# Performance work log

Hardware: AMD Instinct MI355X
Metric: run time of the kernel (lower is better)

## Reference

```python
import jax, jax.numpy as jnp
import numpy as np

T = 4096
V = 88   # visible_dim
H = 512  # hidden_dim
R = 512  # rnn_hidden_dim
REG_FACTOR = 0.2
GIBBS_STEPS = 20
EPS = 1e-6


def setup_inputs() -> dict:
    key = jax.random.key(0)
    ks = jax.random.split(key, 8)
    scale = 1.0 / np.sqrt(H)
    return {
        "visible": (jax.random.uniform(ks[0], (T, V)) < 0.5).astype(jnp.float32),
        "rand_h": jax.random.uniform(ks[1], (T - 1, GIBBS_STEPS, H), dtype=jnp.float32),
        "rand_v": jax.random.uniform(ks[2], (T - 1, GIBBS_STEPS, V), dtype=jnp.float32),
        "w": jax.random.normal(ks[3], (H, V), dtype=jnp.float32) * scale,
        "wuu": jax.random.normal(ks[4], (R, R), dtype=jnp.float32) * scale,
        "wuv": jax.random.normal(ks[5], (V, R), dtype=jnp.float32) * scale,
        "wuh": jax.random.normal(ks[6], (H, R), dtype=jnp.float32) * scale,
        "wvu": jax.random.normal(ks[7], (R, V), dtype=jnp.float32) * scale,
        "bv": jnp.zeros((V,), jnp.float32),
        "bh": jnp.zeros((H,), jnp.float32),
        "bu": jnp.zeros((R,), jnp.float32),
        "u0": jnp.zeros((R,), jnp.float32),
    }


def reference(visible, rand_h, rand_v, w, wuu, wuv, wuh, wvu, bv, bh, bu, u0):
    time_steps = visible.shape[0]
    v_seq = visible[1:]  # v_t for t = 1..T-1, shape [T-1, V]

    # RNN state depends only on data, not on Gibbs samples -> single scan.
    def u_step(u_prev, v_t):
        u_new = jnp.tanh(wvu @ v_t + wuu @ u_prev + bu)
        return u_new, u_prev  # emit u_{t-1} (bias conditioning state)

    _, u_prev = jax.lax.scan(u_step, u0, v_seq)  # [T-1, R]

    # Per-timestep RBM biases (F.linear(u, W, b) = u @ W.T + b).
    bh_t = u_prev @ wuh.T + bh  # [T-1, H]
    bv_t = u_prev @ wuv.T + bv  # [T-1, V]

    # 20 Gibbs steps, batched over all time steps at once.
    def gibbs_step(v, rands):
        rh, rv = rands  # [T-1, H], [T-1, V]
        p_h = jax.nn.sigmoid(v @ w.T + bh_t)
        h = jax.nn.relu(jnp.sign(p_h - rh))         # Bernoulli sample
        p_v = jax.nn.sigmoid(h @ w + bv_t)
        v_new = jax.nn.relu(jnp.sign(p_v - rv))
        return v_new, None

    neg, _ = jax.lax.scan(
        gibbs_step, v_seq,
        (jnp.swapaxes(rand_h, 0, 1), jnp.swapaxes(rand_v, 0, 1)),
    )  # negative samples [T-1, V]

    # Cross-entropy between data and sigmoid(bv_t), summed then /time_steps.
    y_t = jax.nn.sigmoid(bv_t)
    total_cost = jnp.sum(
        -v_seq * jnp.log(EPS + y_t) - (1.0 - v_seq) * jnp.log(EPS + 1.0 - y_t)
    ) / time_steps

    reg_term = (jnp.linalg.norm(wuv) + jnp.linalg.norm(wuh)) * REG_FACTOR
    total_cost = total_cost + reg_term

    mse = jnp.mean(jnp.abs(v_seq - neg), axis=1)  # per-timestep, [T-1]
    return total_cost, mse, reg_term
```

## Files before the change

kernel.cpp:

```cpp
#include <hip/hip_runtime.h>
#include <cstdint>
#include <cstddef>

#define T4096 4096
#define TM1 4095
#define NV 88
#define NH 512
#define NR 512
#define GS 20
#define EPSV 1e-6f

#define U_OFF 0
#define AB_OFF 2096640
#define BV_OFF 4193280
#define SC_OFF 4553640

__device__ __forceinline__ unsigned int agent_load_u32(const unsigned int* p) {
  return __hip_atomic_load(p, __ATOMIC_RELAXED, __HIP_MEMORY_SCOPE_AGENT);
}
__device__ __forceinline__ void agent_store_f32(float* p, float v) {
  __hip_atomic_store(p, v, __ATOMIC_RELAXED, __HIP_MEMORY_SCOPE_AGENT);
}
__device__ __forceinline__ float sigmoidf_(float x) {
  return 1.0f / (1.0f + expf(-x));
}

__device__ __forceinline__ void store_sc0(float* p, float v) {
  asm volatile("global_store_dword %0, %1, off sc0" :: "v"(p), "v"(v) : "memory");
}
__device__ __forceinline__ unsigned load_sc0(const unsigned* p) {
  unsigned r;
  asm volatile("global_load_dword %0, %1, off sc0\n\ts_waitcnt vmcnt(0)"
               : "=v"(r) : "v"(p) : "memory");
  return r;
}

__device__ __forceinline__ unsigned poll_stag_sc0(const unsigned* p) {
  unsigned r0, r1, r2, r3;
  asm volatile(
    "Lp%=:\n\t"
    "global_load_dword %0, %4, off sc0\n\t"
    "s_sleep 1\n\t"
    "global_load_dword %1, %4, off sc0\n\t"
    "s_sleep 1\n\t"
    "global_load_dword %2, %4, off sc0\n\t"
    "s_sleep 1\n\t"
    "global_load_dword %3, %4, off sc0\n\t"
    "s_waitcnt vmcnt(0)\n\t"
    "v_cmp_ne_u32 vcc, -1, %0\n\t"
    "v_cndmask_b32 %3, %3, %0, vcc\n\t"
    "v_cmp_ne_u32 vcc, -1, %1\n\t"
    "v_cndmask_b32 %3, %3, %1, vcc\n\t"
    "v_cmp_ne_u32 vcc, -1, %2\n\t"
    "v_cndmask_b32 %3, %3, %2, vcc\n\t"
    "v_cmp_eq_u32 vcc, -1, %3\n\t"
    "s_cbranch_vccnz Lp%=\n\t"
    : "=&v"(r0), "=&v"(r1), "=&v"(r2), "=&v"(r3)
    : "v"(p) : "vcc", "memory");
  return r3;
}
__device__ __forceinline__ unsigned poll_stag_sys(const unsigned* p) {
  unsigned r0, r1, r2, r3;
  asm volatile(
    "Lq%=:\n\t"
    "global_load_dword %0, %4, off sc0 sc1\n\t"
    "s_sleep 1\n\t"
    "global_load_dword %1, %4, off sc0 sc1\n\t"
    "s_sleep 1\n\t"
    "global_load_dword %2, %4, off sc0 sc1\n\t"
    "s_sleep 1\n\t"
    "global_load_dword %3, %4, off sc0 sc1\n\t"
    "s_waitcnt vmcnt(0)\n\t"
    "v_cmp_ne_u32 vcc, -1, %0\n\t"
    "v_cndmask_b32 %3, %3, %0, vcc\n\t"
    "v_cmp_ne_u32 vcc, -1, %1\n\t"
    "v_cndmask_b32 %3, %3, %1, vcc\n\t"
    "v_cmp_ne_u32 vcc, -1, %2\n\t"
    "v_cndmask_b32 %3, %3, %2, vcc\n\t"
    "v_cmp_eq_u32 vcc, -1, %3\n\t"
    "s_cbranch_vccnz Lq%=\n\t"
    : "=&v"(r0), "=&v"(r1), "=&v"(r2), "=&v"(r3)
    : "v"(p) : "vcc", "memory");
  return r3;
}

__global__ __launch_bounds__(256) void k_a(const float* __restrict__ visible,
                                           const float* __restrict__ wvu,
                                           const float* __restrict__ bu,
                                           float* __restrict__ A) {
  __shared__ float vbuf[NV * 8];
  const int tid = threadIdx.x;
  const int t0 = blockIdx.x * 8;
  for (int idx = tid; idx < NV * 8; idx += 256) {
    int j = idx / NV, v = idx - j * NV;
    int t = t0 + j;
    vbuf[v * 8 + j] = (t < TM1) ? visible[(size_t)(t + 1) * NV + v] : 0.f;
  }
  __syncthreads();
  for (int rr = 0; rr < 2; rr++) {
    int r = tid + rr * 256;
    float b0 = bu[r];
    float acc[8];
#pragma unroll
    for (int j = 0; j < 8; j++) acc[j] = b0;
    const float* wr = wvu + (size_t)r * NV;
    for (int v = 0; v < NV; v++) {
      float wv = wr[v];
#pragma unroll
      for (int j = 0; j < 8; j++) acc[j] = fmaf(wv, vbuf[v * 8 + j], acc[j]);
    }
#pragma unroll
    for (int j = 0; j < 8; j++) {
      int t = t0 + j;
      if (t < TM1) A[(size_t)t * NR + r] = acc[j];
    }
  }
}

__global__ __launch_bounds__(256) void k_r(const float* __restrict__ wuv,
                                           const float* __restrict__ wuh,
                                           float* __restrict__ sc) {
  size_t stride = (size_t)gridDim.x * 256;
  size_t gid = (size_t)blockIdx.x * 256 + threadIdx.x;
  float s1 = 0.f, s2 = 0.f;
  for (size_t i = gid; i < (size_t)NV * NR; i += stride) { float x = wuv[i]; s1 = fmaf(x, x, s1); }
  for (size_t i = gid; i < (size_t)NH * NR; i += stride) { float x = wuh[i]; s2 = fmaf(x, x, s2); }
  for (int off = 32; off > 0; off >>= 1) {
    s1 += __shfl_down(s1, off, 64);
    s2 += __shfl_down(s2, off, 64);
  }
  if ((threadIdx.x & 63) == 0) {
    atomicAdd(&sc[1], s1);
    atomicAdd(&sc[2], s2);
  }
}

__global__ __launch_bounds__(1024, 4) void k_u5(const float* __restrict__ wuu,
                                                const float* __restrict__ A,
                                                const float* __restrict__ u0,
                                                float* __restrict__ U,
                                                unsigned* __restrict__ ub) {
  __shared__ int s_slot;
  __shared__ int s_fast;
  __shared__ float u_lds[NR];
  __shared__ float partials[1024];
  const int tid = threadIdx.x;
  unsigned* claimc = ub + 8;
  unsigned* winner = ub + 16;
  unsigned* hs     = ub + 17;
  unsigned* vd     = ub + 33;

  if (tid == 0) {
    unsigned xcd;
    asm volatile("s_getreg_b32 %0, hwreg(HW_REG_XCC_ID, 0, 4)" : "=s"(xcd));
    xcd &= 7u;
    unsigned c = atomicAdd(&claimc[xcd], 1u);
    int slot = -1;
    if (c < 4u) {
      if (c == 3u) atomicCAS(winner, 0xFFFFFFFFu, xcd);
      unsigned wnr;
      do { wnr = agent_load_u32(winner); } while (wnr == 0xFFFFFFFFu);
      if (wnr == xcd) slot = (int)c;
    }
    s_slot = slot;
  }
  __syncthreads();
  const int slot = s_slot;
  if (slot < 0) return;

  if (tid == 0) {
    int fast = 1;
    for (int round = 0; round < 4 && fast; ++round) {
      unsigned* hw = hs + round * 4;
      store_sc0((float*)&hw[slot], 0.0f);
      for (int o = 0; o < 4; ++o) {
        if (o == slot) continue;
        int ok = 0;
        for (int it = 0; it < 300; ++it) {
          if (load_sc0(&hw[o]) != 0xFFFFFFFFu) { ok = 1; break; }
        }
        if (!ok) fast = 0;
      }
    }
    __hip_atomic_store(&vd[slot], (unsigned)(fast ? 1 : 0),
                       __ATOMIC_RELAXED, __HIP_MEMORY_SCOPE_AGENT);
    for (int o = 0; o < 4; ++o) {
      unsigned v;
      do { v = agent_load_u32(&vd[o]); } while (v == 0xFFFFFFFFu);
      if (v != 1u) fast = 0;
    }
    s_fast = fast;
  }
  __syncthreads();
  const int fast = s_fast;

  const int r_loc = tid & 127;
  const int kc = tid >> 7;
  const int r0 = slot * 128;

  float Wreg[64];
  {
    const float* wr = wuu + (size_t)(r0 + r_loc) * NR + kc * 64;
#pragma unroll
    for (int i = 0; i < 16; i++) ((float4*)Wreg)[i] = ((const float4*)wr)[i];
  }
#pragma unroll
  for (int i = 0; i < 64; i++) asm volatile("" : "+v"(Wreg[i]));

  if (tid < NR) u_lds[tid] = u0[tid];
  if (tid < 128) agent_store_f32(&U[r0 + tid], u0[r0 + tid]);
  float a_cur = (tid < 128) ? A[r0 + tid] : 0.f;
  int pword = -1;
  if (tid >= 128 && tid < 512) {
    int p = tid - 128;
    pword = (p < r0) ? p : p + 128;
  }
  __syncthreads();

  for (int t = 1; t <= TM1 - 1; t++) {
    float acc = 0.f;
    const float* uc = u_lds + kc * 64;
#pragma unroll
    for (int i = 0; i < 64; i += 4) {
      float4 uv = *(const float4*)(uc + i);
      acc = fmaf(Wreg[i],     uv.x, acc);
      acc = fmaf(Wreg[i + 1], uv.y, acc);
      acc = fmaf(Wreg[i + 2], uv.z, acc);
      acc = fmaf(Wreg[i + 3], uv.w, acc);
    }
    partials[kc * 128 + r_loc] = acc;
    __syncthreads();
    if (tid < 128) {
      float s = a_cur;
#pragma unroll
      for (int kk = 0; kk < 8; kk++) s += partials[kk * 128 + tid];
      float val = tanhf(s);
      if (fast) store_sc0(&U[(size_t)t * NR + r0 + tid], val);
      else      agent_store_f32(&U[(size_t)t * NR + r0 + tid], val);
      u_lds[r0 + tid] = val;
      a_cur = A[(size_t)t * NR + r0 + tid];
    } else if (pword >= 0) {
      const unsigned* p = (const unsigned*)(U + (size_t)t * NR) + pword;
      unsigned w = fast ? poll_stag_sc0(p) : poll_stag_sys(p);
      u_lds[pword] = __uint_as_float(w);
    }
    __syncthreads();
  }
}

__global__ __launch_bounds__(256) void k_bh(const float* __restrict__ Uu,
                                            const float* __restrict__ wuh,
                                            const float* __restrict__ wuv,
                                            const float* __restrict__ bh,
                                            const float* __restrict__ bv,
                                            const float* __restrict__ visible,
                                            float* __restrict__ bht,
                                            float* __restrict__ bvt,
                                            float* __restrict__ sc) {
  __shared__ float uT[NR * 20];
  __shared__ float red[256];
  const int tid = threadIdx.x;
  const int t0 = blockIdx.x * 16;
  const int nt = min(16, TM1 - t0);
  for (int idx = tid; idx < 16 * NR; idx += 256) {
    int tt = idx >> 9, k = idx & 511;
    uT[k * 20 + tt] = (tt < nt) ? Uu[(size_t)(t0 + tt) * NR + k] : 0.f;
  }
  __syncthreads();
  const int h1 = tid, h2 = tid + 256;
  const bool hasv = tid < NV;
  float acc1[16], acc2[16], accv[16];
#pragma unroll
  for (int i = 0; i < 16; i++) acc1[i] = acc2[i] = accv[i] = 0.f;
  const float* w1p = wuh + (size_t)h1 * NR;
  const float* w2p = wuh + (size_t)h2 * NR;
  const float* wvp = wuv + (size_t)(hasv ? tid : 0) * NR;
  for (int k = 0; k < NR; k++) {
    float u16[16];
#pragma unroll
    for (int q = 0; q < 4; q++) *(float4*)(u16 + 4 * q) = *(const float4*)(uT + k * 20 + 4 * q);
    float a = w1p[k], b = w2p[k];
    float c = hasv ? wvp[k] : 0.f;
#pragma unroll
    for (int i = 0; i < 16; i++) {
      acc1[i] = fmaf(a, u16[i], acc1[i]);
      acc2[i] = fmaf(b, u16[i], acc2[i]);
      accv[i] = fmaf(c, u16[i], accv[i]);
    }
  }
  float bh1 = bh[h1], bh2 = bh[h2];
#pragma unroll
  for (int i = 0; i < 16; i++) {
    if (i < nt) {
      bht[(size_t)(t0 + i) * NH + h1] = acc1[i] + bh1;
      bht[(size_t)(t0 + i) * NH + h2] = acc2[i] + bh2;
    }
  }
  float ce = 0.f;
  if (hasv) {
    float bvv = bv[tid];
    for (int i = 0; i < nt; i++) {
      float x = accv[i] + bvv;
      bvt[(size_t)(t0 + i) * NV + tid] = x;
      float y = sigmoidf_(x);
      float vs = visible[(size_t)(t0 + i + 1) * NV + tid];
      ce += -vs * logf(EPSV + y) - (1.f - vs) * logf(EPSV + 1.f - y);
    }
  }
  red[tid] = ce;
  __syncthreads();
  for (int s = 128; s > 0; s >>= 1) {
    if (tid < s) red[tid] += red[tid + s];
    __syncthreads();
  }
  if (tid == 0) atomicAdd(&sc[0], red[0]);
}

__global__ __launch_bounds__(256) void k_g(const float* __restrict__ w,
                                           const float* __restrict__ visible,
                                           const float* __restrict__ rand_h,
                                           const float* __restrict__ rand_v,
                                           const float* __restrict__ bht,
                                           const float* __restrict__ bvt,
                                           float* __restrict__ out) {
  __shared__ float vlds[NV * 20];
  __shared__ float hlds[NH * 20];
  const int tid = threadIdx.x;
  const int t0 = blockIdx.x * 16;
  const int nt = min(16, TM1 - t0);
  for (int idx = tid; idx < NV * 16; idx += 256) {
    int j = idx / NV, v = idx - j * NV;
    vlds[v * 20 + j] = (j < nt) ? visible[(size_t)(t0 + j + 1) * NV + v] : 0.f;
  }
  for (int idx = tid; idx < NH * 20; idx += 256) hlds[idx] = 0.f;
  __syncthreads();
  const int h1 = tid, h2 = tid + 256;
  const int tg = tid >> 5, vg = tid & 31;
  const int v0 = vg * 4;
  const bool bact = vg < 22;
  for (int k = 0; k < GS; k++) {
    {
      float acc1[16], acc2[16];
#pragma unroll
      for (int i = 0; i < 16; i++) acc1[i] = acc2[i] = 0.f;
      const float* w1p = w + (size_t)h1 * NV;
      const float* w2p = w + (size_t)h2 * NV;
      for (int v = 0; v < NV; v++) {
        float vv[16];
#pragma unroll
        for (int q = 0; q < 4; q++) *(float4*)(vv + 4 * q) = *(const float4*)(vlds + v * 20 + 4 * q);
        float a = w1p[v], b = w2p[v];
#pragma unroll
        for (int i = 0; i < 16; i++) {
          acc1[i] = fmaf(a, vv[i], acc1[i]);
          acc2[i] = fmaf(b, vv[i], acc2[i]);
        }
      }
#pragma unroll
      for (int i = 0; i < 16; i++) {
        if (i < nt) {
          size_t t = (size_t)(t0 + i);
          float x1 = acc1[i] + bht[t * NH + h1];
          float x2 = acc2[i] + bht[t * NH + h2];
          float p1 = sigmoidf_(x1);
          float p2 = sigmoidf_(x2);
          float r1 = rand_h[(t * GS + k) * NH + h1];
          float r2 = rand_h[(t * GS + k) * NH + h2];
          hlds[h1 * 20 + i] = (p1 > r1) ? 1.f : 0.f;
          hlds[h2 * 20 + i] = (p2 > r2) ? 1.f : 0.f;
        }
      }
    }
    __syncthreads();
    if (bact) {
      float acc[2][4];
#pragma unroll
      for (int a = 0; a < 2; a++)
#pragma unroll
        for (int b = 0; b < 4; b++) acc[a][b] = 0.f;
#pragma unroll 4
      for (int h = 0; h < NH; h++) {
        float2 hv = *(const float2*)(hlds + h * 20 + tg * 2);
        float4 w4 = *(const float4*)(w + (size_t)h * NV + v0);
        acc[0][0] = fmaf(hv.x, w4.x, acc[0][0]);
        acc[0][1] = fmaf(hv.x, w4.y, acc[0][1]);
        acc[0][2] = fmaf(hv.x, w4.z, acc[0][2]);
        acc[0][3] = fmaf(hv.x, w4.w, acc[0][3]);
        acc[1][0] = fmaf(hv.y, w4.x, acc[1][0]);
        acc[1][1] = fmaf(hv.y, w4.y, acc[1][1]);
        acc[1][2] = fmaf(hv.y, w4.z, acc[1][2]);
        acc[1][3] = fmaf(hv.y, w4.w, acc[1][3]);
      }
#pragma unroll
      for (int a = 0; a < 2; a++) {
        int tt = tg * 2 + a;
        if (tt < nt) {
          size_t t = (size_t)(t0 + tt);
#pragma unroll
          for (int i = 0; i < 4; i++) {
            int v = v0 + i;
            float x = acc[a][i] + bvt[t * NV + v];
            float p = sigmoidf_(x);
            float r = rand_v[(t * GS + k) * NV + v];
            vlds[v * 20 + tt] = (p > r) ? 1.f : 0.f;
          }
        }
      }
    }
    __syncthreads();
  }
  if (tid < 16 && tid < nt) {
    int tt = tid;
    float s = 0.f;
    for (int v = 0; v < NV; v++) {
      float vs = visible[(size_t)(t0 + tt + 1) * NV + v];
      s += fabsf(vs - vlds[v * 20 + tt]);
    }
    out[1 + t0 + tt] = s / 88.f;
  }
}

__global__ void k_f(const float* __restrict__ sc, float* __restrict__ out) {
  float reg = 0.2f * (sqrtf(sc[1]) + sqrtf(sc[2]));
  out[0] = sc[0] / 4096.f + reg;
  out[4096] = reg;
}

extern "C" void kernel_launch(void* const* d_in, const int* in_sizes, int n_in,
                              void* d_out, int out_size, void* d_ws, size_t ws_size,
                              hipStream_t stream) {
  const float* visible = (const float*)d_in[0];
  const float* rand_h  = (const float*)d_in[1];
  const float* rand_v  = (const float*)d_in[2];
  const float* w       = (const float*)d_in[3];
  const float* wuu     = (const float*)d_in[4];
  const float* wuv     = (const float*)d_in[5];
  const float* wuh     = (const float*)d_in[6];
  const float* wvu     = (const float*)d_in[7];
  const float* bv      = (const float*)d_in[8];
  const float* bh      = (const float*)d_in[9];
  const float* bu      = (const float*)d_in[10];
  const float* u0      = (const float*)d_in[11];
  float* out = (float*)d_out;
  float* ws = (float*)d_ws;

  float* Uarr = ws + U_OFF;
  float* Aarr = ws + AB_OFF;
  float* bht  = ws + AB_OFF;
  float* bvt  = ws + BV_OFF;
  float* sc   = ws + SC_OFF;
  unsigned* ub = (unsigned*)sc;

  hipMemsetAsync(Uarr, 0xFF, (size_t)TM1 * NR * sizeof(float), stream);
  hipMemsetAsync(sc, 0, 64, stream);
  hipMemsetAsync((char*)sc + 64, 0xFF, 96, stream);

  k_a<<<512, 256, 0, stream>>>(visible, wvu, bu, Aarr);
  k_r<<<64, 256, 0, stream>>>(wuv, wuh, sc);
  k_u5<<<64, 1024, 0, stream>>>(wuu, Aarr, u0, Uarr, ub);
  k_bh<<<256, 256, 0, stream>>>(Uarr, wuh, wuv, bh, bv, visible, bht, bvt, sc);
  k_g<<<256, 256, 0, stream>>>(w, visible, rand_h, rand_v, bht, bvt, out);
  k_f<<<1, 1, 0, stream>>>(sc, out);
}
```

Measured before the change: 6.424 ms.

## Split RNN recurrence across eight 512-thread blocks with per-wave polling

The sequential tanh recurrence kernel now spreads the 512 hidden rows over eight cooperating blocks on one XCD (64 rows each) instead of four blocks of 128 rows, each with 512 threads. Each wave owns a 64-wide slice of u: it either takes its own previous value or polls the published U row for that slice, writes it to LDS, and computes its partial dot product immediately. Double-buffered partials cut the per-step barriers from two to one. The intent is lower per-step latency on the serial critical path, at the cost of more inter-block polling traffic and a handshake across eight participants.

```diff
diff --git a/kernel.cpp b/kernel.cpp
--- a/kernel.cpp
+++ b/kernel.cpp
@@ -135,20 +135,20 @@
   }
 }
 
-__global__ __launch_bounds__(1024, 4) void k_u5(const float* __restrict__ wuu,
-                                                const float* __restrict__ A,
-                                                const float* __restrict__ u0,
-                                                float* __restrict__ U,
-                                                unsigned* __restrict__ ub) {
+__global__ __launch_bounds__(512, 2) void k_u6(const float* __restrict__ wuu,
+                                               const float* __restrict__ A,
+                                               const float* __restrict__ u0,
+                                               float* __restrict__ U,
+                                               unsigned* __restrict__ ub) {
   __shared__ int s_slot;
   __shared__ int s_fast;
-  __shared__ float u_lds[NR];
-  __shared__ float partials[1024];
+  __shared__ float u_buf[NR];
+  __shared__ float partials[2 * NR];
   const int tid = threadIdx.x;
   unsigned* claimc = ub + 8;
   unsigned* winner = ub + 16;
   unsigned* hs     = ub + 17;
-  unsigned* vd     = ub + 33;
+  unsigned* vd     = ub + 49;
 
   if (tid == 0) {
     unsigned xcd;
@@ -156,8 +156,8 @@
     xcd &= 7u;
     unsigned c = atomicAdd(&claimc[xcd], 1u);
     int slot = -1;
-    if (c < 4u) {
-      if (c == 3u) atomicCAS(winner, 0xFFFFFFFFu, xcd);
+    if (c < 8u) {
+      if (c == 7u) atomicCAS(winner, 0xFFFFFFFFu, xcd);
       unsigned wnr;
       do { wnr = agent_load_u32(winner); } while (wnr == 0xFFFFFFFFu);
       if (wnr == xcd) slot = (int)c;
@@ -171,9 +171,9 @@
   if (tid == 0) {
     int fast = 1;
     for (int round = 0; round < 4 && fast; ++round) {
-      unsigned* hw = hs + round * 4;
+      unsigned* hw = hs + round * 8;
       store_sc0((float*)&hw[slot], 0.0f);
-      for (int o = 0; o < 4; ++o) {
+      for (int o = 0; o < 8; ++o) {
         if (o == slot) continue;
         int ok = 0;
         for (int it = 0; it < 300; ++it) {
@@ -184,7 +184,7 @@
     }
     __hip_atomic_store(&vd[slot], (unsigned)(fast ? 1 : 0),
                        __ATOMIC_RELAXED, __HIP_MEMORY_SCOPE_AGENT);
-    for (int o = 0; o < 4; ++o) {
+    for (int o = 0; o < 8; ++o) {
       unsigned v;
       do { v = agent_load_u32(&vd[o]); } while (v == 0xFFFFFFFFu);
       if (v != 1u) fast = 0;
@@ -194,58 +194,73 @@
   __syncthreads();
   const int fast = s_fast;
 
-  const int r_loc = tid & 127;
-  const int kc = tid >> 7;
-  const int r0 = slot * 128;
+  const int lane = tid & 63;
+  const int wv   = tid >> 6;
+  const int r0   = slot * 64;
+  const int chunk = (wv == 0) ? slot : ((wv - 1 < slot) ? (wv - 1) : wv);
+  float* ubw = u_buf + chunk * 64;
 
   float Wreg[64];
   {
-    const float* wr = wuu + (size_t)(r0 + r_loc) * NR + kc * 64;
-#pragma unroll
-    for (int i = 0; i < 16; i++) ((float4*)Wreg)[i] = ((const float4*)wr)[i];
+    const float* wr = wuu + (size_t)(r0 + lane) * NR + chunk * 64;
+#pragma unroll
+    for (int i = 0; i < 16; i++) {
+      float4 w4 = ((const float4*)wr)[i];
+      Wreg[4 * i]     = w4.x;
+      Wreg[4 * i + 1] = w4.y;
+      Wreg[4 * i + 2] = w4.z;
+      Wreg[4 * i + 3] = w4.w;
+    }
   }
 #pragma unroll
   for (int i = 0; i < 64; i++) asm volatile("" : "+v"(Wreg[i]));
 
-  if (tid < NR) u_lds[tid] = u0[tid];
-  if (tid < 128) agent_store_f32(&U[r0 + tid], u0[r0 + tid]);
-  float a_cur = (tid < 128) ? A[r0 + tid] : 0.f;
-  int pword = -1;
-  if (tid >= 128 && tid < 512) {
-    int p = tid - 128;
-    pword = (p < r0) ? p : p + 128;
-  }
-  __syncthreads();
-
-  for (int t = 1; t <= TM1 - 1; t++) {
-    float acc = 0.f;
-    const float* uc = u_lds + kc * 64;
-#pragma unroll
-    for (int i = 0; i < 64; i += 4) {
-      float4 uv = *(const float4*)(uc + i);
-      acc = fmaf(Wreg[i],     uv.x, acc);
-      acc = fmaf(Wreg[i + 1], uv.y, acc);
-      acc = fmaf(Wreg[i + 2], uv.z, acc);
-      acc = fmaf(Wreg[i + 3], uv.w, acc);
-    }
-    partials[kc * 128 + r_loc] = acc;
-    __syncthreads();
-    if (tid < 128) {
-      float s = a_cur;
-#pragma unroll
-      for (int kk = 0; kk < 8; kk++) s += partials[kk * 128 + tid];
-      float val = tanhf(s);
-      if (fast) store_sc0(&U[(size_t)t * NR + r0 + tid], val);
-      else      agent_store_f32(&U[(size_t)t * NR + r0 + tid], val);
-      u_lds[r0 + tid] = val;
-      a_cur = A[(size_t)t * NR + r0 + tid];
-    } else if (pword >= 0) {
-      const unsigned* p = (const unsigned*)(U + (size_t)t * NR) + pword;
+  float val = 0.f, a_cur = 0.f;
+  if (wv == 0) {
+    agent_store_f32(&U[r0 + lane], u0[r0 + lane]);
+    a_cur = A[r0 + lane];
+  }
+
+#define KU_STEP(T_, UVAL_) do {                                                  \
+    ubw[lane] = (UVAL_);                                                         \
+    float acc = 0.f;                                                             \
+    _Pragma("unroll")                                                            \
+    for (int i = 0; i < 64; i += 4) {                                            \
+      float4 uv = *(const float4*)(ubw + i);                                     \
+      acc = fmaf(Wreg[i],     uv.x, acc);                                        \
+      acc = fmaf(Wreg[i + 1], uv.y, acc);                                        \
+      acc = fmaf(Wreg[i + 2], uv.z, acc);                                        \
+      acc = fmaf(Wreg[i + 3], uv.w, acc);                                        \
+    }                                                                            \
+    partials[((T_) & 1) * NR + chunk * 64 + lane] = acc;                         \
+    __syncthreads();                                                             \
+    if (wv == 0) {                                                               \
+      float s = a_cur;                                                           \
+      _Pragma("unroll")                                                          \
+      for (int kk = 0; kk < 8; kk++) s += partials[((T_) & 1) * NR + kk * 64 + lane]; \
+      val = tanhf(s);                                                            \
+      if (fast) store_sc0(&U[(size_t)(T_) * NR + r0 + lane], val);               \
+      else      agent_store_f32(&U[(size_t)(T_) * NR + r0 + lane], val);         \
+      a_cur = A[(size_t)(T_) * NR + r0 + lane];       \
+    }                                                                            \
+  } while (0)
+
+  {
+    float u_val = u0[chunk * 64 + lane];
+    KU_STEP(1, u_val);
+  }
+  for (int t = 2; t <= TM1 - 1; t++) {
+    float u_val;
+    if (wv == 0) {
+      u_val = val;
+    } else {
+      const unsigned* p = (const unsigned*)(U + (size_t)(t - 1) * NR) + chunk * 64 + lane;
       unsigned w = fast ? poll_stag_sc0(p) : poll_stag_sys(p);
-      u_lds[pword] = __uint_as_float(w);
-    }
-    __syncthreads();
-  }
+      u_val = __uint_as_float(w);
+    }
+    KU_STEP(t, u_val);
+  }
+#undef KU_STEP
 }
 
 __global__ __launch_bounds__(256) void k_bh(const float* __restrict__ Uu,
@@ -453,11 +468,11 @@
 
   hipMemsetAsync(Uarr, 0xFF, (size_t)TM1 * NR * sizeof(float), stream);
   hipMemsetAsync(sc, 0, 64, stream);
-  hipMemsetAsync((char*)sc + 64, 0xFF, 96, stream);
+  hipMemsetAsync((char*)sc + 64, 0xFF, 192, stream);
 
   k_a<<<512, 256, 0, stream>>>(visible, wvu, bu, Aarr);
   k_r<<<64, 256, 0, stream>>>(wuv, wuh, sc);
-  k_u5<<<64, 1024, 0, stream>>>(wuu, Aarr, u0, Uarr, ub);
+  k_u6<<<64, 512, 0, stream>>>(wuu, Aarr, u0, Uarr, ub);
   k_bh<<<256, 256, 0, stream>>>(Uarr, wuh, wuv, bh, bv, visible, bht, bvt, sc);
   k_g<<<256, 256, 0, stream>>>(w, visible, rand_h, rand_v, bht, bvt, out);
   k_f<<<1, 1, 0, stream>>>(sc, out);
```

Measured after the change: 6.795 ms. 1.06x slower.
